# Optimization experiments

Hardware: AMD Instinct MI355X
Metric: run time of the kernel (lower is better)

The kernel has to match this reference:

```python
import jax, jax.numpy as jnp
import numpy as np

NUM_HEADS = 8
GROUP = 16
LN_EPS = 1e-5

def _star_relu(x, scale, bias):
    return scale * jnp.square(jax.nn.relu(x)) + bias

def _layernorm(x, w, b):
    mu = x.mean(-1, keepdims=True)
    var = jnp.mean(jnp.square(x - mu), -1, keepdims=True)
    return (x - mu) / jnp.sqrt(var + LN_EPS) * w + b

def _attention(x, qkv_w, proj_w, proj_b, pa_scale, pa_bias, lf_w, lf_b, hf_w, hf_b, lf_gamma, hf_gamma):
    B, N, C = x.shape
    hd = C // NUM_HEADS
    detail = _star_relu(x, pa_scale, pa_bias)
    lf = jnp.tanh(detail @ lf_w.T + lf_b)                      # (B,N,H)
    hf = jax.nn.softplus(detail @ hf_w.T + hf_b)
    hf_sq = jnp.square(hf)
    hf = 2.0 * hf_sq / (hf_sq + 0.3678)
    lf = jnp.repeat(lf, hd, axis=-1)                           # (B,N,C): per-head value repeated across head_dim
    hf = jnp.repeat(hf, hd, axis=-1)
    qkv = (x @ qkv_w.T).reshape(B, N, 3, NUM_HEADS, hd).transpose(2, 0, 3, 1, 4)
    q, k, v = qkv[0], qkv[1], qkv[2]
    q = q * (hd ** -0.5)
    attn = jax.nn.softmax(jnp.einsum('bhqd,bhkd->bhqk', q, k), axis=-1)
    attn_out = jnp.einsum('bhqk,bhkd->bhqd', attn, v).transpose(0, 2, 1, 3).reshape(B, N, C)
    value_tokens = v.transpose(0, 2, 1, 3).reshape(B, N, C)
    high_res = value_tokens - attn_out
    attn_out = attn_out + attn_out * lf * lf_gamma + hf * high_res * hf_gamma
    return attn_out @ proj_w.T + proj_b

def _freq_scale(x, rw1_w, rw1_scale, rw1_bias, rw2_w, freq_w):
    # x: (B,C,H,W); freq_w: (num_filters, C//group, base_size, base_size//2+1) == rfft grid
    B, C, H, W = x.shape
    xf = jnp.fft.rfft2(x, axes=(2, 3), norm='ortho')           # (B,C,fh,fw) complex
    pooled = x.mean(axis=(2, 3))                               # (B,C)
    h = _star_relu(pooled @ rw1_w.T, rw1_scale, rw1_bias)
    routing = jnp.tanh((h @ rw2_w.T).reshape(B, GROUP, -1))    # (B,g,f)
    fh, fw = xf.shape[2], xf.shape[3]
    dyn = jnp.einsum('bgf,fchw->bgchw', routing, freq_w).reshape(B, C, fh, fw)
    xf = xf * dyn
    return jnp.fft.irfft2(xf, s=(H, W), axes=(2, 3), norm='ortho')

def _forward(x, norm1_w, norm1_b, qkv_w, proj_w, proj_b, pa_scale, pa_bias, lf_w, lf_b, hf_w, hf_b,
             lf_gamma, hf_gamma, fs1_rw1_w, fs1_rw1_scale, fs1_rw1_bias, fs1_rw2_w, fs1_fw, gamma_1,
             norm2_w, norm2_b, fc1_w, fc1_b, fc2_w, fc2_b, fs2_rw1_w, fs2_rw1_scale, fs2_rw1_bias,
             fs2_rw2_w, fs2_fw, gamma_2):
    B, C, H, W = x.shape
    tokens = x.reshape(B, C, H * W).transpose(0, 2, 1)         # nchw -> nlc
    att_tokens = _attention(_layernorm(tokens, norm1_w, norm1_b),
                            qkv_w, proj_w, proj_b, pa_scale, pa_bias,
                            lf_w, lf_b, hf_w, hf_b, lf_gamma, hf_gamma)
    att_feat = att_tokens.transpose(0, 2, 1).reshape(B, C, H, W)
    att_feat = _freq_scale(att_feat, fs1_rw1_w, fs1_rw1_scale, fs1_rw1_bias, fs1_rw2_w, fs1_fw) + att_feat
    att_tokens = att_feat.reshape(B, C, H * W).transpose(0, 2, 1)
    tokens = tokens + gamma_1 * att_tokens
    h = _layernorm(tokens, norm2_w, norm2_b)
    mlp_tokens = jax.nn.gelu(h @ fc1_w.T + fc1_b, approximate=False) @ fc2_w.T + fc2_b
    mlp_feat = mlp_tokens.transpose(0, 2, 1).reshape(B, C, H, W)
    mlp_feat = _freq_scale(mlp_feat, fs2_rw1_w, fs2_rw1_scale, fs2_rw1_bias, fs2_rw2_w, fs2_fw) + mlp_feat
    mlp_tokens = mlp_feat.reshape(B, C, H * W).transpose(0, 2, 1)
    tokens = tokens + gamma_2 * mlp_tokens
    return tokens.transpose(0, 2, 1).reshape(B, C, H, W)

def setup_inputs() -> dict:
    key = jax.random.key(0)
    ks = jax.random.split(key, 16)
    B, C, H, W = 16, 512, 32, 32
    heads, group, nf, bs = 8, 16, 4, 32
    hid_rw = int(C * 0.125)
    hid_mlp = int(C * 4.0)
    bfs = bs // 2 + 1
    d = {}
    d['x'] = jax.random.normal(ks[0], (B, C, H, W), jnp.float32)
    d['norm1_w'] = jnp.ones((C,), jnp.float32); d['norm1_b'] = jnp.zeros((C,), jnp.float32)
    d['qkv_w'] = jax.random.normal(ks[1], (3 * C, C), jnp.float32) * 0.02
    d['proj_w'] = jax.random.normal(ks[2], (C, C), jnp.float32) * 0.02
    d['proj_b'] = jnp.zeros((C,), jnp.float32)
    d['pa_scale'] = jnp.ones((1,), jnp.float32); d['pa_bias'] = jnp.zeros((1,), jnp.float32)
    d['lf_w'] = jax.random.normal(ks[3], (heads, C), jnp.float32) * 0.02
    d['lf_b'] = jnp.zeros((heads,), jnp.float32)
    d['hf_w'] = jax.random.normal(ks[4], (heads, C), jnp.float32) * 0.02
    d['hf_b'] = jnp.zeros((heads,), jnp.float32)
    d['lf_gamma'] = 1e-5 * jnp.ones((C,), jnp.float32)
    d['hf_gamma'] = 1e-5 * jnp.ones((C,), jnp.float32)
    d['fs1_rw1_w'] = jax.random.normal(ks[5], (hid_rw, C), jnp.float32) * 0.02
    d['fs1_rw1_scale'] = jnp.ones((1,), jnp.float32); d['fs1_rw1_bias'] = jnp.zeros((1,), jnp.float32)
    d['fs1_rw2_w'] = jax.random.normal(ks[6], (group * nf, hid_rw), jnp.float32) * 0.02
    d['fs1_fw'] = jax.random.normal(ks[7], (nf, C // group, bs, bfs), jnp.float32) * 1e-5
    d['gamma_1'] = 1e-4 * jnp.ones((C,), jnp.float32)
    d['norm2_w'] = jnp.ones((C,), jnp.float32); d['norm2_b'] = jnp.zeros((C,), jnp.float32)
    d['fc1_w'] = jax.random.normal(ks[8], (hid_mlp, C), jnp.float32) * 0.02
    d['fc1_b'] = jnp.zeros((hid_mlp,), jnp.float32)
    d['fc2_w'] = jax.random.normal(ks[9], (C, hid_mlp), jnp.float32) * 0.02
    d['fc2_b'] = jnp.zeros((C,), jnp.float32)
    d['fs2_rw1_w'] = jax.random.normal(ks[10], (hid_rw, C), jnp.float32) * 0.02
    d['fs2_rw1_scale'] = jnp.ones((1,), jnp.float32); d['fs2_rw1_bias'] = jnp.zeros((1,), jnp.float32)
    d['fs2_rw2_w'] = jax.random.normal(ks[11], (group * nf, hid_rw), jnp.float32) * 0.02
    d['fs2_fw'] = jax.random.normal(ks[12], (nf, C // group, bs, bfs), jnp.float32) * 1e-5
    d['gamma_2'] = 1e-4 * jnp.ones((C,), jnp.float32)
    return d

def reference(x, norm1_w, norm1_b, qkv_w, proj_w, proj_b, pa_scale, pa_bias, lf_w, lf_b, hf_w, hf_b,
              lf_gamma, hf_gamma, fs1_rw1_w, fs1_rw1_scale, fs1_rw1_bias, fs1_rw2_w, fs1_fw, gamma_1,
              norm2_w, norm2_b, fc1_w, fc1_b, fc2_w, fc2_b, fs2_rw1_w, fs2_rw1_scale, fs2_rw1_bias,
              fs2_rw2_w, fs2_fw, gamma_2):
    return _forward(x, norm1_w, norm1_b, qkv_w, proj_w, proj_b, pa_scale, pa_bias, lf_w, lf_b, hf_w, hf_b,
                    lf_gamma, hf_gamma, fs1_rw1_w, fs1_rw1_scale, fs1_rw1_bias, fs1_rw2_w, fs1_fw, gamma_1,
                    norm2_w, norm2_b, fc1_w, fc1_b, fc2_w, fc2_b, fs2_rw1_w, fs2_rw1_scale, fs2_rw1_bias,
                    fs2_rw2_w, fs2_fw, gamma_2)
```

## Files before the change

kernel.cpp:

```cpp
#include <hip/hip_runtime.h>
#include <cstdint>
#include <cstddef>

#define B_   16
#define C_   512
#define N_   1024
#define M_   (B_*N_)
#define NH_  8
#define HD_  64
#define C3_  1536
#define CH_  2048

typedef __attribute__((ext_vector_type(8))) short bf16x8;
typedef __attribute__((ext_vector_type(4))) float f32x4;
typedef __attribute__((ext_vector_type(4))) unsigned short u16x4;

__device__ __forceinline__ unsigned short f2bf(float f) {
  union { float f; unsigned u; } v; v.f = f;
  unsigned r = v.u + 0x7fffu + ((v.u >> 16) & 1u);
  return (unsigned short)(r >> 16);
}
__device__ __forceinline__ float bf2f(unsigned short h) {
  union { unsigned u; float f; } v; v.u = ((unsigned)h) << 16;
  return v.f;
}
__device__ __forceinline__ unsigned f2u(float f) {
  union { float f; unsigned u; } v; v.f = f; return v.u;
}

__global__ __launch_bounds__(256) void k_f2b4(
    const float* __restrict__ s0, unsigned short* __restrict__ d0,
    const float* __restrict__ s1, unsigned short* __restrict__ d1,
    const float* __restrict__ s2, unsigned short* __restrict__ d2,
    const float* __restrict__ s3, unsigned short* __restrict__ d3) {
  int blk = blockIdx.x, t = threadIdx.x;
  const float* s; unsigned short* d; int off;
  if (blk < 3072)      { s = s0; d = d0; off = blk * 256; }
  else if (blk < 4096) { s = s1; d = d1; off = (blk - 3072) * 256; }
  else if (blk < 8192) { s = s2; d = d2; off = (blk - 4096) * 256; }
  else                 { s = s3; d = d3; off = (blk - 8192) * 256; }
  int i = off + t;
  d[i] = f2bf(s[i]);
}

__global__ __launch_bounds__(256) void k_twid(unsigned short* __restrict__ gtab) {
  int idx = blockIdx.x * 256 + threadIdx.x;
  if (idx >= 6400) return;
  int tab = idx / 1280, rem = idx % 1280;
  int i = rem / 40, j = rem % 40;
  float v = 0.f;
  if (j < 32) {
    float th = 0.19634954084936207f * (float)((i * j) & 31);
    float s, c;
    __sincosf(th, &s, &c);
    if (tab == 0) v = c;
    else if (tab == 1) v = s;
    else if (tab == 2) v = -s;
    else {
      float wg = (j == 0 || j == 16) ? 1.f : 2.f;
      if (j >= 17) wg = 0.f;
      v = (tab == 3) ? wg * c : -wg * s;
    }
  }
  gtab[idx] = f2bf(v);
}

__global__ __launch_bounds__(256) void k_transpose_cn(const float* __restrict__ x,
                                                      float* __restrict__ tok) {
  __shared__ float s[32][33];
  const int n0 = blockIdx.x * 32, c0 = blockIdx.y * 32, b = blockIdx.z;
  const int j = threadIdx.x & 31, i0 = threadIdx.x >> 5;
  #pragma unroll
  for (int k = 0; k < 4; ++k) {
    int i = i0 + k * 8;
    s[i][j] = x[(size_t)(b * C_ + c0 + i) * N_ + n0 + j];
  }
  __syncthreads();
  #pragma unroll
  for (int k = 0; k < 4; ++k) {
    int i = i0 + k * 8;
    tok[(size_t)(b * N_ + n0 + i) * C_ + c0 + j] = s[j][i];
  }
}

template<bool WITH>
__global__ __launch_bounds__(256) void k_ln(const float* __restrict__ tok,
    const float* __restrict__ w, const float* __restrict__ bia,
    const float* __restrict__ lfw, const float* __restrict__ lfb,
    const float* __restrict__ hfw, const float* __restrict__ hfb,
    const float* __restrict__ pa_s, const float* __restrict__ pa_b,
    unsigned short* __restrict__ lnout, float* __restrict__ lfout,
    float* __restrict__ hfout) {
  const int t = threadIdx.x, wv = t >> 6, l = t & 63;
  const int row = blockIdx.x * 4 + wv;
  const float* p = tok + (size_t)row * C_;
  float v[8];
  *(float4*)&v[0] = *(const float4*)(p + 4 * l);
  *(float4*)&v[4] = *(const float4*)(p + 256 + 4 * l);
  float s = 0.f, q = 0.f;
  #pragma unroll
  for (int i = 0; i < 8; ++i) { s += v[i]; q += v[i] * v[i]; }
  #pragma unroll
  for (int off = 1; off < 64; off <<= 1) { s += __shfl_xor(s, off); q += __shfl_xor(q, off); }
  float mu = s * (1.f / 512.f);
  float var = q * (1.f / 512.f) - mu * mu;
  float rstd = rsqrtf(var + 1e-5f);
  float wv8[8], bv8[8];
  *(float4*)&wv8[0] = *(const float4*)(w + 4 * l);
  *(float4*)&wv8[4] = *(const float4*)(w + 256 + 4 * l);
  *(float4*)&bv8[0] = *(const float4*)(bia + 4 * l);
  *(float4*)&bv8[4] = *(const float4*)(bia + 256 + 4 * l);
  float ln[8];
  #pragma unroll
  for (int i = 0; i < 8; ++i) ln[i] = (v[i] - mu) * rstd * wv8[i] + bv8[i];
  u16x4 o0 = { f2bf(ln[0]), f2bf(ln[1]), f2bf(ln[2]), f2bf(ln[3]) };
  u16x4 o1 = { f2bf(ln[4]), f2bf(ln[5]), f2bf(ln[6]), f2bf(ln[7]) };
  *(u16x4*)(lnout + (size_t)row * C_ + 4 * l) = o0;
  *(u16x4*)(lnout + (size_t)row * C_ + 256 + 4 * l) = o1;
  if (WITH) {
    float ps = pa_s[0], pb = pa_b[0];
    float d[8];
    #pragma unroll
    for (int i = 0; i < 8; ++i) { float r = fmaxf(ln[i], 0.f); d[i] = ps * r * r + pb; }
    float lacc[8], hacc[8];
    #pragma unroll
    for (int h = 0; h < 8; ++h) {
      float lw[8], hw[8];
      *(float4*)&lw[0] = *(const float4*)(lfw + h * C_ + 4 * l);
      *(float4*)&lw[4] = *(const float4*)(lfw + h * C_ + 256 + 4 * l);
      *(float4*)&hw[0] = *(const float4*)(hfw + h * C_ + 4 * l);
      *(float4*)&hw[4] = *(const float4*)(hfw + h * C_ + 256 + 4 * l);
      float la = 0.f, ha = 0.f;
      #pragma unroll
      for (int i = 0; i < 8; ++i) { la += d[i] * lw[i]; ha += d[i] * hw[i]; }
      lacc[h] = la; hacc[h] = ha;
    }
    #pragma unroll
    for (int h = 0; h < 8; ++h)
      #pragma unroll
      for (int off = 1; off < 64; off <<= 1) {
        lacc[h] += __shfl_xor(lacc[h], off);
        hacc[h] += __shfl_xor(hacc[h], off);
      }
    float lv = lacc[0], hv = hacc[0];
    #pragma unroll
    for (int h = 1; h < 8; ++h) { if (l == h) { lv = lacc[h]; hv = hacc[h]; } }
    if (l < 8) {
      lfout[(size_t)row * 8 + l] = tanhf(lv + lfb[l]);
      float z = hv + hfb[l];
      float sp = (z > 15.f) ? z : log1pf(__expf(z));
      float s2 = sp * sp;
      hfout[(size_t)row * 8 + l] = 2.f * s2 / (s2 + 0.3678f);
    }
  }
}

template<int EPI>
__global__ __launch_bounds__(256) void k_gemm(const unsigned short* __restrict__ A,
    const unsigned short* __restrict__ Bt, const float* __restrict__ bias,
    void* __restrict__ outv, unsigned short* __restrict__ vtg, int Nn, int K) {
  __shared__ __align__(16) unsigned short Asm[128 * 40];
  __shared__ __align__(16) unsigned short Bsm[128 * 40];
  const int t = threadIdx.x, w = t >> 6, l = t & 63;
  const int lane15 = l & 15, quad = l >> 4;
  const int n0 = blockIdx.x * 128, m0 = blockIdx.y * 128;
  const int wm = w >> 1, wn = w & 1;
  f32x4 acc[4][4];
  #pragma unroll
  for (int i = 0; i < 4; ++i)
    #pragma unroll
    for (int j = 0; j < 4; ++j) acc[i][j] = (f32x4){0.f, 0.f, 0.f, 0.f};
  const int sr = t >> 2, sc = (t & 3) * 8;
  const unsigned short* Ab = A + (size_t)(m0 + sr) * K + sc;
  const unsigned short* Bb = Bt + (size_t)(n0 + sr) * K + sc;
  const size_t rstep = (size_t)64 * K;
  bf16x8 ga0 = *(const bf16x8*)Ab;
  bf16x8 ga1 = *(const bf16x8*)(Ab + rstep);
  bf16x8 gb0 = *(const bf16x8*)Bb;
  bf16x8 gb1 = *(const bf16x8*)(Bb + rstep);
  for (int k0 = 0; k0 < K; k0 += 32) {
    __syncthreads();
    *(bf16x8*)&Asm[sr * 40 + sc] = ga0;
    *(bf16x8*)&Asm[(sr + 64) * 40 + sc] = ga1;
    *(bf16x8*)&Bsm[sr * 40 + sc] = gb0;
    *(bf16x8*)&Bsm[(sr + 64) * 40 + sc] = gb1;
    __syncthreads();
    if (k0 + 32 < K) {
      ga0 = *(const bf16x8*)(Ab + k0 + 32);
      ga1 = *(const bf16x8*)(Ab + rstep + k0 + 32);
      gb0 = *(const bf16x8*)(Bb + k0 + 32);
      gb1 = *(const bf16x8*)(Bb + rstep + k0 + 32);
    }
    bf16x8 af[4], bg[4];
    #pragma unroll
    for (int i = 0; i < 4; ++i)
      af[i] = *(const bf16x8*)&Asm[(wm * 64 + i * 16 + lane15) * 40 + quad * 8];
    #pragma unroll
    for (int i = 0; i < 4; ++i)
      bg[i] = *(const bf16x8*)&Bsm[(wn * 64 + i * 16 + lane15) * 40 + quad * 8];
    #pragma unroll
    for (int i = 0; i < 4; ++i)
      #pragma unroll
      for (int j = 0; j < 4; ++j)
        acc[i][j] = __builtin_amdgcn_mfma_f32_16x16x32_bf16(af[i], bg[j], acc[i][j], 0, 0, 0);
  }
  #pragma unroll
  for (int i = 0; i < 4; ++i) {
    int grow = m0 + wm * 64 + i * 16 + quad * 4;
    int bq = grow >> 10, nq = grow & 1023;
    #pragma unroll
    for (int j = 0; j < 4; ++j) {
      int gcol = n0 + wn * 64 + j * 16 + lane15;
      float bs = (EPI == 0) ? 0.f : bias[gcol];
      if (EPI == 1 || EPI == 3) {
        float4 o = make_float4(acc[i][j][0] + bs, acc[i][j][1] + bs,
                               acc[i][j][2] + bs, acc[i][j][3] + bs);
        *(float4*)&((float*)outv)[((size_t)(bq * C_ + gcol) << 10) + nq] = o;
      } else if (EPI == 0) {
        u16x4 pv;
        #pragma unroll
        for (int r = 0; r < 4; ++r) {
          unsigned short hv = f2bf(acc[i][j][r]);
          pv[r] = hv;
          ((unsigned short*)outv)[(size_t)(grow + r) * Nn + gcol] = hv;
        }
        if (gcol >= 1024)
          *(u16x4*)&vtg[((size_t)(bq * C_ + gcol - 1024) << 10) + nq] = pv;
      } else {
        #pragma unroll
        for (int r = 0; r < 4; ++r) {
          float vv = acc[i][j][r] + bs;
          float e = __builtin_amdgcn_exp2f(-(2.302118073f * vv +
                                             0.1029455568f * vv * vv * vv));
          float g = vv * __builtin_amdgcn_rcpf(1.f + e);
          ((unsigned short*)outv)[(size_t)(grow + r) * Nn + gcol] = f2bf(g);
        }
      }
    }
  }
}

__global__ __launch_bounds__(256) void k_flash(const unsigned short* __restrict__ qkv,
    const unsigned short* __restrict__ vtg, const float* __restrict__ lf,
    const float* __restrict__ hf, const float* __restrict__ lgam,
    const float* __restrict__ hgam, unsigned short* __restrict__ y) {
  const int t = threadIdx.x, w = t >> 6, l = t & 63;
  const int lane15 = l & 15, quad = l >> 4;
  const int q0 = blockIdx.x * 64;
  const int h = blockIdx.y, b = blockIdx.z;
  __shared__ __align__(16) unsigned short kt[128 * 72];
  __shared__ __align__(16) unsigned short vt[64 * 136];
  __shared__ __align__(16) unsigned short pl[4][16 * 72];

  bf16x8 aq0, aq1;
  {
    const unsigned short* qp = qkv + (size_t)(b * N_ + q0 + w * 16 + lane15) * C3_ + h * 64 + quad * 8;
    bf16x8 r0 = *(const bf16x8*)qp;
    bf16x8 r1 = *(const bf16x8*)(qp + 32);
    #pragma unroll
    for (int i = 0; i < 8; ++i) {
      aq0[i] = (short)f2bf(0.1803368801111713f * bf2f((unsigned short)r0[i]));
      aq1[i] = (short)f2bf(0.1803368801111713f * bf2f((unsigned short)r1[i]));
    }
  }
  f32x4 O[4];
  #pragma unroll
  for (int i = 0; i < 4; ++i) O[i] = (f32x4){0.f, 0.f, 0.f, 0.f};
  float lsum = 0.f;

  const int sr = t >> 3;
  const int sc = (t & 7) * 8;
  const unsigned short* kb = qkv + (size_t)(b * N_ + sr) * C3_ + 512 + h * 64 + sc;
  const unsigned short* vb = vtg + (size_t)((b * NH_ + h) * HD_ + sr) * N_ + sc;
  bf16x8 gk0 = *(const bf16x8*)kb;
  bf16x8 gk1 = *(const bf16x8*)(kb + (size_t)32 * C3_);
  bf16x8 gk2 = *(const bf16x8*)(kb + (size_t)64 * C3_);
  bf16x8 gk3 = *(const bf16x8*)(kb + (size_t)96 * C3_);
  bf16x8 gv0 = *(const bf16x8*)vb;
  bf16x8 gv1 = *(const bf16x8*)(vb + 64);
  bf16x8 gv2 = *(const bf16x8*)(vb + 32 * N_);
  bf16x8 gv3 = *(const bf16x8*)(vb + 32 * N_ + 64);

  for (int kti = 0; kti < 8; ++kti) {
    __syncthreads();
    *(bf16x8*)&kt[sr * 72 + sc] = gk0;
    *(bf16x8*)&kt[(sr + 32) * 72 + sc] = gk1;
    *(bf16x8*)&kt[(sr + 64) * 72 + sc] = gk2;
    *(bf16x8*)&kt[(sr + 96) * 72 + sc] = gk3;
    *(bf16x8*)&vt[sr * 136 + sc] = gv0;
    *(bf16x8*)&vt[sr * 136 + 64 + sc] = gv1;
    *(bf16x8*)&vt[(sr + 32) * 136 + sc] = gv2;
    *(bf16x8*)&vt[(sr + 32) * 136 + 64 + sc] = gv3;
    __syncthreads();
    if (kti < 7) {
      const unsigned short* kn = kb + (size_t)((kti + 1) * 128) * C3_;
      const unsigned short* vn = vb + (kti + 1) * 128;
      gk0 = *(const bf16x8*)kn;
      gk1 = *(const bf16x8*)(kn + (size_t)32 * C3_);
      gk2 = *(const bf16x8*)(kn + (size_t)64 * C3_);
      gk3 = *(const bf16x8*)(kn + (size_t)96 * C3_);
      gv0 = *(const bf16x8*)vn;
      gv1 = *(const bf16x8*)(vn + 64);
      gv2 = *(const bf16x8*)(vn + 32 * N_);
      gv3 = *(const bf16x8*)(vn + 32 * N_ + 64);
    }

    #pragma unroll
    for (int half = 0; half < 2; ++half) {
      f32x4 S[4];
      #pragma unroll
      for (int nt = 0; nt < 4; ++nt) {
        const int nrow = half * 64 + nt * 16 + lane15;
        bf16x8 ak0 = *(const bf16x8*)&kt[nrow * 72 + quad * 8];
        bf16x8 ak1 = *(const bf16x8*)&kt[nrow * 72 + 32 + quad * 8];
        f32x4 z = (f32x4){0.f, 0.f, 0.f, 0.f};
        z = __builtin_amdgcn_mfma_f32_16x16x32_bf16(ak0, aq0, z, 0, 0, 0);
        z = __builtin_amdgcn_mfma_f32_16x16x32_bf16(ak1, aq1, z, 0, 0, 0);
        S[nt] = z;
      }
      #pragma unroll
      for (int nt = 0; nt < 4; ++nt)
        #pragma unroll
        for (int r = 0; r < 4; ++r) {
          float pv = __builtin_amdgcn_exp2f(S[nt][r]);
          S[nt][r] = pv;
          lsum += pv;
        }
      #pragma unroll
      for (int nt = 0; nt < 4; ++nt) {
        unsigned lo = __builtin_amdgcn_perm(f2u(S[nt][1]), f2u(S[nt][0]), 0x07060302u);
        unsigned hi = __builtin_amdgcn_perm(f2u(S[nt][3]), f2u(S[nt][2]), 0x07060302u);
        uint2 pk = make_uint2(lo, hi);
        *(uint2*)&pl[w][lane15 * 72 + nt * 16 + quad * 4] = pk;
      }
      #pragma unroll
      for (int nc = 0; nc < 2; ++nc) {
        bf16x8 ap = *(const bf16x8*)&pl[w][lane15 * 72 + nc * 32 + quad * 8];
        #pragma unroll
        for (int dt = 0; dt < 4; ++dt) {
          bf16x8 bv = *(const bf16x8*)&vt[(dt * 16 + lane15) * 136 + half * 64 + nc * 32 + quad * 8];
          O[dt] = __builtin_amdgcn_mfma_f32_16x16x32_bf16(ap, bv, O[dt], 0, 0, 0);
        }
      }
    }
  }

  lsum += __shfl_xor(lsum, 16);
  lsum += __shfl_xor(lsum, 32);
  float inv = 1.f / lsum;
  float invr[4], lfr[4], hfr[4];
  #pragma unroll
  for (int r = 0; r < 4; ++r) {
    invr[r] = __shfl(inv, quad * 4 + r);
    int grow = b * N_ + q0 + w * 16 + quad * 4 + r;
    lfr[r] = lf[grow * 8 + h];
    hfr[r] = hf[grow * 8 + h];
  }
  const size_t rowb = (size_t)(b * N_ + q0 + w * 16 + quad * 4);
  #pragma unroll
  for (int dt = 0; dt < 4; ++dt) {
    int cc = h * 64 + dt * 16 + lane15;
    float lg = lgam[cc], hg = hgam[cc];
    #pragma unroll
    for (int r = 0; r < 4; ++r) {
      float a = O[dt][r] * invr[r];
      float vval = bf2f(qkv[(rowb + r) * C3_ + 1024 + cc]);
      float res = a + a * lfr[r] * lg + hfr[r] * (vval - a) * hg;
      y[(rowb + r) * C_ + cc] = f2bf(res);
    }
  }
}

__global__ __launch_bounds__(256) void k_pool(const float* __restrict__ feat,
                                              float* __restrict__ pooled) {
  int row = blockIdx.x * 4 + (threadIdx.x >> 6);
  int l = threadIdx.x & 63;
  const float4* p = (const float4*)(feat + (size_t)row * N_);
  float4 a = p[l], b4 = p[l + 64], c4 = p[l + 128], d4 = p[l + 192];
  float s = a.x + a.y + a.z + a.w + b4.x + b4.y + b4.z + b4.w +
            c4.x + c4.y + c4.z + c4.w + d4.x + d4.y + d4.z + d4.w;
  #pragma unroll
  for (int off = 1; off < 64; off <<= 1) s += __shfl_xor(s, off);
  if (l == 0) pooled[row] = s * (1.f / 1024.f);
}

__global__ __launch_bounds__(256) void k_routing(const float* __restrict__ pooled,
    const float* __restrict__ rw1, const float* __restrict__ rw1s,
    const float* __restrict__ rw1b, const float* __restrict__ rw2,
    float* __restrict__ routing) {
  const int b = blockIdx.x, t = threadIdx.x;
  __shared__ float plds[512];
  __shared__ float tile[64][65];
  __shared__ float hl[64];
  plds[t] = pooled[b * 512 + t];
  plds[t + 256] = pooled[b * 512 + t + 256];
  __syncthreads();
  float acc = 0.f;
  for (int c0 = 0; c0 < 512; c0 += 64) {
    #pragma unroll
    for (int kk = 0; kk < 16; ++kk) {
      int idx = kk * 256 + t;
      tile[idx >> 6][idx & 63] = rw1[(size_t)(idx >> 6) * 512 + c0 + (idx & 63)];
    }
    __syncthreads();
    if (t < 64) {
      #pragma unroll
      for (int i = 0; i < 64; ++i) acc += plds[c0 + i] * tile[t][i];
    }
    __syncthreads();
  }
  if (t < 64) {
    float r = fmaxf(acc, 0.f);
    hl[t] = rw1s[0] * r * r + rw1b[0];
  }
  __syncthreads();
  if (t < 64) {
    float r2 = 0.f;
    #pragma unroll
    for (int j = 0; j < 64; ++j) r2 += hl[j] * rw2[(size_t)t * 64 + j];
    routing[b * 64 + t] = tanhf(r2);
  }
}

__global__ __launch_bounds__(256) void k_freq(const float* __restrict__ feat,
    const float* __restrict__ routing, const float* __restrict__ fwtab,
    const unsigned short* __restrict__ gtab, float* __restrict__ enh) {
  const int c = blockIdx.x, b = blockIdx.y, t = threadIdx.x;
  const int g = c >> 5, cc = c & 31;
  const int w = t >> 6, l = t & 63;
  const int lane15 = l & 15, quad = l >> 4;
  const int mt = w & 1, nt = w >> 1;
  __shared__ __align__(16) unsigned short Xbf[32 * 40];
  __shared__ __align__(16) float p[32 * 36];
  __shared__ __align__(16) unsigned short Tabs[6400];
  __shared__ __align__(16) unsigned short pl1r[32 * 40], pl1i[32 * 40];
  __shared__ __align__(16) unsigned short pl2r[32 * 40], pl2i[32 * 40];
  __shared__ __align__(16) unsigned short pl3r[32 * 40], pl3i[32 * 40];
  __shared__ float Ms[1024];
  const size_t base = (size_t)(b * C_ + c) * N_;

  {
    float4 v = ((const float4*)(feat + base))[t];
    int hh = t >> 3, w4 = (t & 7) * 4;
    *(float4*)&p[hh * 36 + w4] = v;
    u16x4 xb = { f2bf(v.x), f2bf(v.y), f2bf(v.z), f2bf(v.w) };
    *(u16x4*)&Xbf[hh * 40 + w4] = xb;
  }
  {
    const uint4* src = (const uint4*)gtab;
    uint4* dst = (uint4*)Tabs;
    #pragma unroll
    for (int k = 0; k < 4; ++k) {
      int o = k * 256 + t;
      if (o < 800) dst[o] = src[o];
    }
  }
  {
    float r0 = routing[b * 64 + g * 4 + 0];
    float r1 = routing[b * 64 + g * 4 + 1];
    float r2 = routing[b * 64 + g * 4 + 2];
    float r3 = routing[b * 64 + g * 4 + 3];
    const float* fb = fwtab + (size_t)cc * 544;
    #pragma unroll
    for (int k = 0; k < 4; ++k) {
      int o = k * 256 + t;
      int fh = o >> 5, fw = o & 31;
      float mv = 0.f;
      if (fw < 17) {
        int fi = fh * 17 + fw;
        mv = (r0 * fb[fi] + r1 * fb[17408 + fi] + r2 * fb[34816 + fi] +
              r3 * fb[52224 + fi]) * (1.f / 1024.f);
      }
      Ms[o] = mv;
    }
  }
  __syncthreads();

  const unsigned short* Tc  = Tabs;
  const unsigned short* Ts  = Tabs + 1280;
  const unsigned short* Tsn = Tabs + 2560;
  const unsigned short* Tcw = Tabs + 3840;
  const unsigned short* Tsw = Tabs + 5120;
  const int arow = (mt * 16 + lane15) * 40 + quad * 8;
  const int brow = (nt * 16 + lane15) * 40 + quad * 8;
  const int prow = (nt * 16 + lane15) * 40 + mt * 16 + quad * 4;
  const f32x4 zz = (f32x4){0.f, 0.f, 0.f, 0.f};

  {
    bf16x8 aX = *(const bf16x8*)&Xbf[arow];
    bf16x8 bC = *(const bf16x8*)&Tc[brow];
    bf16x8 bS = *(const bf16x8*)&Tsn[brow];
    f32x4 re = __builtin_amdgcn_mfma_f32_16x16x32_bf16(aX, bC, zz, 0, 0, 0);
    f32x4 im = __builtin_amdgcn_mfma_f32_16x16x32_bf16(aX, bS, zz, 0, 0, 0);
    uint2 pr = make_uint2(__builtin_amdgcn_perm(f2u(re[1]), f2u(re[0]), 0x07060302u),
                          __builtin_amdgcn_perm(f2u(re[3]), f2u(re[2]), 0x07060302u));
    uint2 pi = make_uint2(__builtin_amdgcn_perm(f2u(im[1]), f2u(im[0]), 0x07060302u),
                          __builtin_amdgcn_perm(f2u(im[3]), f2u(im[2]), 0x07060302u));
    *(uint2*)&pl1r[prow] = pr;
    *(uint2*)&pl1i[prow] = pi;
  }
  __syncthreads();
  {
    bf16x8 aC = *(const bf16x8*)&Tc[arow];
    bf16x8 aS = *(const bf16x8*)&Ts[arow];
    bf16x8 aN = *(const bf16x8*)&Tsn[arow];
    bf16x8 bR = *(const bf16x8*)&pl1r[brow];
    bf16x8 bI = *(const bf16x8*)&pl1i[brow];
    f32x4 er = __builtin_amdgcn_mfma_f32_16x16x32_bf16(aC, bR, zz, 0, 0, 0);
    er = __builtin_amdgcn_mfma_f32_16x16x32_bf16(aS, bI, er, 0, 0, 0);
    f32x4 ei = __builtin_amdgcn_mfma_f32_16x16x32_bf16(aC, bI, zz, 0, 0, 0);
    ei = __builtin_amdgcn_mfma_f32_16x16x32_bf16(aN, bR, ei, 0, 0, 0);
    #pragma unroll
    for (int r = 0; r < 4; ++r) {
      float mk = Ms[(mt * 16 + quad * 4 + r) * 32 + nt * 16 + lane15];
      er[r] *= mk; ei[r] *= mk;
    }
    uint2 pr = make_uint2(__builtin_amdgcn_perm(f2u(er[1]), f2u(er[0]), 0x07060302u),
                          __builtin_amdgcn_perm(f2u(er[3]), f2u(er[2]), 0x07060302u));
    uint2 pi = make_uint2(__builtin_amdgcn_perm(f2u(ei[1]), f2u(ei[0]), 0x07060302u),
                          __builtin_amdgcn_perm(f2u(ei[3]), f2u(ei[2]), 0x07060302u));
    *(uint2*)&pl2r[prow] = pr;
    *(uint2*)&pl2i[prow] = pi;
  }
  __syncthreads();
  {
    bf16x8 aR = *(const bf16x8*)&pl2r[arow];
    bf16x8 aI = *(const bf16x8*)&pl2i[arow];
    bf16x8 bC = *(const bf16x8*)&Tc[brow];
    bf16x8 bS = *(const bf16x8*)&Ts[brow];
    bf16x8 bN = *(const bf16x8*)&Tsn[brow];
    f32x4 zr = __builtin_amdgcn_mfma_f32_16x16x32_bf16(aR, bC, zz, 0, 0, 0);
    zr = __builtin_amdgcn_mfma_f32_16x16x32_bf16(aI, bN, zr, 0, 0, 0);
    f32x4 zi = __builtin_amdgcn_mfma_f32_16x16x32_bf16(aI, bC, zz, 0, 0, 0);
    zi = __builtin_amdgcn_mfma_f32_16x16x32_bf16(aR, bS, zi, 0, 0, 0);
    uint2 pr = make_uint2(__builtin_amdgcn_perm(f2u(zr[1]), f2u(zr[0]), 0x07060302u),
                          __builtin_amdgcn_perm(f2u(zr[3]), f2u(zr[2]), 0x07060302u));
    uint2 pi = make_uint2(__builtin_amdgcn_perm(f2u(zi[1]), f2u(zi[0]), 0x07060302u),
                          __builtin_amdgcn_perm(f2u(zi[3]), f2u(zi[2]), 0x07060302u));
    *(uint2*)&pl3r[prow] = pr;
    *(uint2*)&pl3i[prow] = pi;
  }
  __syncthreads();
  {
    bf16x8 aC = *(const bf16x8*)&Tcw[arow];
    bf16x8 aS = *(const bf16x8*)&Tsw[arow];
    bf16x8 bR = *(const bf16x8*)&pl3r[brow];
    bf16x8 bI = *(const bf16x8*)&pl3i[brow];
    f32x4 y = __builtin_amdgcn_mfma_f32_16x16x32_bf16(aC, bR, zz, 0, 0, 0);
    y = __builtin_amdgcn_mfma_f32_16x16x32_bf16(aS, bI, y, 0, 0, 0);
    int hh = nt * 16 + lane15, w0 = mt * 16 + quad * 4;
    float4 res = *(const float4*)&p[hh * 36 + w0];
    float4 o = make_float4(y[0] + res.x, y[1] + res.y, y[2] + res.z, y[3] + res.w);
    *(float4*)&enh[base + hh * 32 + w0] = o;
  }
}

__global__ __launch_bounds__(256) void k_add_t(const float* __restrict__ enh,
    const float* __restrict__ gamma, float* __restrict__ tok) {
  __shared__ float s[32][33];
  const int n0 = blockIdx.x * 32, c0 = blockIdx.y * 32, b = blockIdx.z;
  const int j = threadIdx.x & 31, i0 = threadIdx.x >> 5;
  #pragma unroll
  for (int k = 0; k < 4; ++k) {
    int i = i0 + k * 8;
    s[i][j] = enh[(size_t)(b * C_ + c0 + i) * N_ + n0 + j];
  }
  __syncthreads();
  float gv = gamma[c0 + j];
  #pragma unroll
  for (int k = 0; k < 4; ++k) {
    int i = i0 + k * 8;
    size_t o = (size_t)(b * N_ + n0 + i) * C_ + c0 + j;
    tok[o] += gv * s[j][i];
  }
}

__global__ __launch_bounds__(256) void k_final(const float* __restrict__ tok,
    const float* __restrict__ gamma, const float* __restrict__ enh,
    float* __restrict__ out) {
  __shared__ float s[32][33];
  const int n0 = blockIdx.x * 32, c0 = blockIdx.y * 32, b = blockIdx.z;
  const int j = threadIdx.x & 31, i0 = threadIdx.x >> 5;
  #pragma unroll
  for (int k = 0; k < 4; ++k) {
    int i = i0 + k * 8;
    s[i][j] = tok[(size_t)(b * N_ + n0 + i) * C_ + c0 + j];
  }
  __syncthreads();
  #pragma unroll
  for (int k = 0; k < 4; ++k) {
    int i = i0 + k * 8;
    size_t o = (size_t)(b * C_ + c0 + i) * N_ + n0 + j;
    out[o] = s[j][i] + gamma[c0 + i] * enh[o];
  }
}

extern "C" void kernel_launch(void* const* d_in, const int* in_sizes, int n_in,
                              void* d_out, int out_size, void* d_ws, size_t ws_size,
                              hipStream_t stream) {
  (void)in_sizes; (void)n_in; (void)out_size; (void)ws_size;
  const float* x      = (const float*)d_in[0];
  const float* n1w    = (const float*)d_in[1];
  const float* n1b    = (const float*)d_in[2];
  const float* qkv_w  = (const float*)d_in[3];
  const float* proj_w = (const float*)d_in[4];
  const float* proj_b = (const float*)d_in[5];
  const float* pa_s   = (const float*)d_in[6];
  const float* pa_b   = (const float*)d_in[7];
  const float* lf_w   = (const float*)d_in[8];
  const float* lf_b   = (const float*)d_in[9];
  const float* hf_w   = (const float*)d_in[10];
  const float* hf_b   = (const float*)d_in[11];
  const float* lf_g   = (const float*)d_in[12];
  const float* hf_g   = (const float*)d_in[13];
  const float* f1rw1w = (const float*)d_in[14];
  const float* f1rw1s = (const float*)d_in[15];
  const float* f1rw1b = (const float*)d_in[16];
  const float* f1rw2w = (const float*)d_in[17];
  const float* f1fw   = (const float*)d_in[18];
  const float* gamma1 = (const float*)d_in[19];
  const float* n2w    = (const float*)d_in[20];
  const float* n2b    = (const float*)d_in[21];
  const float* fc1w   = (const float*)d_in[22];
  const float* fc1b   = (const float*)d_in[23];
  const float* fc2w   = (const float*)d_in[24];
  const float* fc2b   = (const float*)d_in[25];
  const float* f2rw1w = (const float*)d_in[26];
  const float* f2rw1s = (const float*)d_in[27];
  const float* f2rw1b = (const float*)d_in[28];
  const float* f2rw2w = (const float*)d_in[29];
  const float* f2fw   = (const float*)d_in[30];
  const float* gamma2 = (const float*)d_in[31];

  char* ws = (char*)d_ws;
  float*          tokens = (float*)(ws + 0);
  float*          f1buf  = (float*)(ws + 33554432ULL);
  float*          f2buf  = (float*)(ws + 67108864ULL);
  float*          f3buf  = (float*)(ws + 100663296ULL);
  unsigned short* regA   = (unsigned short*)(ws + 134217728ULL);
  unsigned short* abuf   = (unsigned short*)(ws + 201326592ULL);
  float*          lfbuf  = (float*)(ws + 218103808ULL);
  float*          hfbuf  = (float*)(ws + 218628096ULL);
  float*          pooled = (float*)(ws + 219152384ULL);
  float*          routing= (float*)(ws + 219185152ULL);
  unsigned short* wq     = (unsigned short*)(ws + 219189248ULL);
  unsigned short* wp     = (unsigned short*)(ws + 220762112ULL);
  unsigned short* w1     = (unsigned short*)(ws + 221286400ULL);
  unsigned short* w2     = (unsigned short*)(ws + 223383552ULL);
  unsigned short* gtab   = (unsigned short*)(ws + 225480704ULL);
  unsigned short* vtg    = (unsigned short*)f1buf;

  k_f2b4<<<12288, 256, 0, stream>>>(qkv_w, wq, proj_w, wp, fc1w, w1, fc2w, w2);
  k_twid<<<25, 256, 0, stream>>>(gtab);

  k_transpose_cn<<<dim3(32, 16, 16), 256, 0, stream>>>(x, tokens);
  k_ln<true><<<4096, 256, 0, stream>>>(tokens, n1w, n1b, lf_w, lf_b, hf_w, hf_b,
                                       pa_s, pa_b, abuf, lfbuf, hfbuf);
  k_gemm<0><<<dim3(12, 128), 256, 0, stream>>>(abuf, wq, n1b, regA, vtg, C3_, C_);
  k_flash<<<dim3(16, 8, 16), 256, 0, stream>>>(regA, vtg, lfbuf, hfbuf, lf_g, hf_g, abuf);
  k_gemm<1><<<dim3(4, 128), 256, 0, stream>>>(abuf, wp, proj_b, f2buf, nullptr, C_, C_);
  k_pool<<<2048, 256, 0, stream>>>(f2buf, pooled);
  k_routing<<<16, 256, 0, stream>>>(pooled, f1rw1w, f1rw1s, f1rw1b, f1rw2w, routing);
  k_freq<<<dim3(512, 16), 256, 0, stream>>>(f2buf, routing, f1fw, gtab, f3buf);
  k_add_t<<<dim3(32, 16, 16), 256, 0, stream>>>(f3buf, gamma1, tokens);
  k_ln<false><<<4096, 256, 0, stream>>>(tokens, n2w, n2b, nullptr, nullptr, nullptr,
                                        nullptr, nullptr, nullptr, abuf, nullptr, nullptr);
  k_gemm<2><<<dim3(16, 128), 256, 0, stream>>>(abuf, w1, fc1b, regA, nullptr, CH_, C_);
  k_gemm<3><<<dim3(4, 128), 256, 0, stream>>>(regA, w2, fc2b, f2buf, nullptr, C_, CH_);
  k_pool<<<2048, 256, 0, stream>>>(f2buf, pooled);
  k_routing<<<16, 256, 0, stream>>>(pooled, f2rw1w, f2rw1s, f2rw1b, f2rw2w, routing);
  k_freq<<<dim3(512, 16), 256, 0, stream>>>(f2buf, routing, f2fw, gtab, f3buf);
  k_final<<<dim3(32, 16, 16), 256, 0, stream>>>(tokens, gamma2, f3buf, (float*)d_out);
}
```

Before: 548.9 us.

## Keep residual stream in channel-major layout and fuse transposes into LN and freq kernels

```diff
diff --git a/kernel.cpp b/kernel.cpp
--- a/kernel.cpp
+++ b/kernel.cpp
@@ -65,92 +65,86 @@
   gtab[idx] = f2bf(v);
 }
 
-__global__ __launch_bounds__(256) void k_transpose_cn(const float* __restrict__ x,
-                                                      float* __restrict__ tok) {
-  __shared__ float s[32][33];
-  const int n0 = blockIdx.x * 32, c0 = blockIdx.y * 32, b = blockIdx.z;
-  const int j = threadIdx.x & 31, i0 = threadIdx.x >> 5;
-  #pragma unroll
-  for (int k = 0; k < 4; ++k) {
-    int i = i0 + k * 8;
-    s[i][j] = x[(size_t)(b * C_ + c0 + i) * N_ + n0 + j];
-  }
-  __syncthreads();
-  #pragma unroll
-  for (int k = 0; k < 4; ++k) {
-    int i = i0 + k * 8;
-    tok[(size_t)(b * N_ + n0 + i) * C_ + c0 + j] = s[j][i];
-  }
-}
-
 template<bool WITH>
-__global__ __launch_bounds__(256) void k_ln(const float* __restrict__ tok,
+__global__ __launch_bounds__(256) void k_lnt(const float* __restrict__ src,
     const float* __restrict__ w, const float* __restrict__ bia,
     const float* __restrict__ lfw, const float* __restrict__ lfb,
     const float* __restrict__ hfw, const float* __restrict__ hfb,
     const float* __restrict__ pa_s, const float* __restrict__ pa_b,
     unsigned short* __restrict__ lnout, float* __restrict__ lfout,
     float* __restrict__ hfout) {
+  __shared__ unsigned short s[512 * 34];
   const int t = threadIdx.x, wv = t >> 6, l = t & 63;
-  const int row = blockIdx.x * 4 + wv;
-  const float* p = tok + (size_t)row * C_;
-  float v[8];
-  *(float4*)&v[0] = *(const float4*)(p + 4 * l);
-  *(float4*)&v[4] = *(const float4*)(p + 256 + 4 * l);
-  float s = 0.f, q = 0.f;
-  #pragma unroll
-  for (int i = 0; i < 8; ++i) { s += v[i]; q += v[i] * v[i]; }
-  #pragma unroll
-  for (int off = 1; off < 64; off <<= 1) { s += __shfl_xor(s, off); q += __shfl_xor(q, off); }
-  float mu = s * (1.f / 512.f);
-  float var = q * (1.f / 512.f) - mu * mu;
-  float rstd = rsqrtf(var + 1e-5f);
+  const int n0 = blockIdx.x * 32, b = blockIdx.y;
+  const int cl = t >> 3;
+  const int nn = (t & 7) * 4;
+  #pragma unroll
+  for (int k = 0; k < 16; ++k) {
+    int c = k * 32 + cl;
+    float4 v = *(const float4*)&src[(size_t)(b * C_ + c) * N_ + n0 + nn];
+    s[c * 34 + nn]     = f2bf(v.x);
+    s[c * 34 + nn + 1] = f2bf(v.y);
+    s[c * 34 + nn + 2] = f2bf(v.z);
+    s[c * 34 + nn + 3] = f2bf(v.w);
+  }
+  __syncthreads();
   float wv8[8], bv8[8];
-  *(float4*)&wv8[0] = *(const float4*)(w + 4 * l);
-  *(float4*)&wv8[4] = *(const float4*)(w + 256 + 4 * l);
-  *(float4*)&bv8[0] = *(const float4*)(bia + 4 * l);
-  *(float4*)&bv8[4] = *(const float4*)(bia + 256 + 4 * l);
-  float ln[8];
-  #pragma unroll
-  for (int i = 0; i < 8; ++i) ln[i] = (v[i] - mu) * rstd * wv8[i] + bv8[i];
-  u16x4 o0 = { f2bf(ln[0]), f2bf(ln[1]), f2bf(ln[2]), f2bf(ln[3]) };
-  u16x4 o1 = { f2bf(ln[4]), f2bf(ln[5]), f2bf(ln[6]), f2bf(ln[7]) };
-  *(u16x4*)(lnout + (size_t)row * C_ + 4 * l) = o0;
-  *(u16x4*)(lnout + (size_t)row * C_ + 256 + 4 * l) = o1;
-  if (WITH) {
-    float ps = pa_s[0], pb = pa_b[0];
-    float d[8];
-    #pragma unroll
-    for (int i = 0; i < 8; ++i) { float r = fmaxf(ln[i], 0.f); d[i] = ps * r * r + pb; }
-    float lacc[8], hacc[8];
-    #pragma unroll
-    for (int h = 0; h < 8; ++h) {
-      float lw[8], hw[8];
-      *(float4*)&lw[0] = *(const float4*)(lfw + h * C_ + 4 * l);
-      *(float4*)&lw[4] = *(const float4*)(lfw + h * C_ + 256 + 4 * l);
-      *(float4*)&hw[0] = *(const float4*)(hfw + h * C_ + 4 * l);
-      *(float4*)&hw[4] = *(const float4*)(hfw + h * C_ + 256 + 4 * l);
-      float la = 0.f, ha = 0.f;
-      #pragma unroll
-      for (int i = 0; i < 8; ++i) { la += d[i] * lw[i]; ha += d[i] * hw[i]; }
-      lacc[h] = la; hacc[h] = ha;
-    }
-    #pragma unroll
-    for (int h = 0; h < 8; ++h)
-      #pragma unroll
-      for (int off = 1; off < 64; off <<= 1) {
-        lacc[h] += __shfl_xor(lacc[h], off);
-        hacc[h] += __shfl_xor(hacc[h], off);
+  #pragma unroll
+  for (int k = 0; k < 8; ++k) { wv8[k] = w[l + 64 * k]; bv8[k] = bia[l + 64 * k]; }
+  float ps = 1.f, pb = 0.f;
+  if (WITH) { ps = pa_s[0]; pb = pa_b[0]; }
+  for (int ri = 0; ri < 8; ++ri) {
+    const int n = wv * 8 + ri;
+    const int row = b * N_ + n0 + n;
+    float v[8];
+    #pragma unroll
+    for (int k = 0; k < 8; ++k) v[k] = bf2f(s[(l + 64 * k) * 34 + n]);
+    float sm = 0.f, q = 0.f;
+    #pragma unroll
+    for (int k = 0; k < 8; ++k) { sm += v[k]; q += v[k] * v[k]; }
+    #pragma unroll
+    for (int off = 1; off < 64; off <<= 1) { sm += __shfl_xor(sm, off); q += __shfl_xor(q, off); }
+    float mu = sm * (1.f / 512.f);
+    float var = q * (1.f / 512.f) - mu * mu;
+    float rstd = rsqrtf(var + 1e-5f);
+    float ln[8];
+    #pragma unroll
+    for (int k = 0; k < 8; ++k) ln[k] = (v[k] - mu) * rstd * wv8[k] + bv8[k];
+    #pragma unroll
+    for (int k = 0; k < 8; ++k)
+      lnout[(size_t)row * C_ + l + 64 * k] = f2bf(ln[k]);
+    if (WITH) {
+      float d[8];
+      #pragma unroll
+      for (int k = 0; k < 8; ++k) { float r = fmaxf(ln[k], 0.f); d[k] = ps * r * r + pb; }
+      float lacc[8], hacc[8];
+      #pragma unroll
+      for (int h = 0; h < 8; ++h) {
+        float la = 0.f, ha = 0.f;
+        #pragma unroll
+        for (int k = 0; k < 8; ++k) {
+          la += d[k] * lfw[h * C_ + l + 64 * k];
+          ha += d[k] * hfw[h * C_ + l + 64 * k];
+        }
+        lacc[h] = la; hacc[h] = ha;
       }
-    float lv = lacc[0], hv = hacc[0];
-    #pragma unroll
-    for (int h = 1; h < 8; ++h) { if (l == h) { lv = lacc[h]; hv = hacc[h]; } }
-    if (l < 8) {
-      lfout[(size_t)row * 8 + l] = tanhf(lv + lfb[l]);
-      float z = hv + hfb[l];
-      float sp = (z > 15.f) ? z : log1pf(__expf(z));
-      float s2 = sp * sp;
-      hfout[(size_t)row * 8 + l] = 2.f * s2 / (s2 + 0.3678f);
+      #pragma unroll
+      for (int h = 0; h < 8; ++h)
+        #pragma unroll
+        for (int off = 1; off < 64; off <<= 1) {
+          lacc[h] += __shfl_xor(lacc[h], off);
+          hacc[h] += __shfl_xor(hacc[h], off);
+        }
+      float lv = lacc[0], hv = hacc[0];
+      #pragma unroll
+      for (int h = 1; h < 8; ++h) { if (l == h) { lv = lacc[h]; hv = hacc[h]; } }
+      if (l < 8) {
+        lfout[(size_t)row * 8 + l] = tanhf(lv + lfb[l]);
+        float z = hv + hfb[l];
+        float sp = (z > 15.f) ? z : log1pf(__expf(z));
+        float s2 = sp * sp;
+        hfout[(size_t)row * 8 + l] = 2.f * s2 / (s2 + 0.3678f);
+      }
     }
   }
 }
@@ -424,7 +418,8 @@
 
 __global__ __launch_bounds__(256) void k_freq(const float* __restrict__ feat,
     const float* __restrict__ routing, const float* __restrict__ fwtab,
-    const unsigned short* __restrict__ gtab, float* __restrict__ enh) {
+    const unsigned short* __restrict__ gtab, const float* __restrict__ res,
+    const float* __restrict__ gamma, float* __restrict__ outp) {
   const int c = blockIdx.x, b = blockIdx.y, t = threadIdx.x;
   const int g = c >> 5, cc = c & 31;
   const int w = t >> 6, l = t & 63;
@@ -549,49 +544,12 @@
     f32x4 y = __builtin_amdgcn_mfma_f32_16x16x32_bf16(aC, bR, zz, 0, 0, 0);
     y = __builtin_amdgcn_mfma_f32_16x16x32_bf16(aS, bI, y, 0, 0, 0);
     int hh = nt * 16 + lane15, w0 = mt * 16 + quad * 4;
-    float4 res = *(const float4*)&p[hh * 36 + w0];
-    float4 o = make_float4(y[0] + res.x, y[1] + res.y, y[2] + res.z, y[3] + res.w);
-    *(float4*)&enh[base + hh * 32 + w0] = o;
-  }
-}
-
-__global__ __launch_bounds__(256) void k_add_t(const float* __restrict__ enh,
-    const float* __restrict__ gamma, float* __restrict__ tok) {
-  __shared__ float s[32][33];
-  const int n0 = blockIdx.x * 32, c0 = blockIdx.y * 32, b = blockIdx.z;
-  const int j = threadIdx.x & 31, i0 = threadIdx.x >> 5;
-  #pragma unroll
-  for (int k = 0; k < 4; ++k) {
-    int i = i0 + k * 8;
-    s[i][j] = enh[(size_t)(b * C_ + c0 + i) * N_ + n0 + j];
-  }
-  __syncthreads();
-  float gv = gamma[c0 + j];
-  #pragma unroll
-  for (int k = 0; k < 4; ++k) {
-    int i = i0 + k * 8;
-    size_t o = (size_t)(b * N_ + n0 + i) * C_ + c0 + j;
-    tok[o] += gv * s[j][i];
-  }
-}
-
-__global__ __launch_bounds__(256) void k_final(const float* __restrict__ tok,
-    const float* __restrict__ gamma, const float* __restrict__ enh,
-    float* __restrict__ out) {
-  __shared__ float s[32][33];
-  const int n0 = blockIdx.x * 32, c0 = blockIdx.y * 32, b = blockIdx.z;
-  const int j = threadIdx.x & 31, i0 = threadIdx.x >> 5;
-  #pragma unroll
-  for (int k = 0; k < 4; ++k) {
-    int i = i0 + k * 8;
-    s[i][j] = tok[(size_t)(b * N_ + n0 + i) * C_ + c0 + j];
-  }
-  __syncthreads();
-  #pragma unroll
-  for (int k = 0; k < 4; ++k) {
-    int i = i0 + k * 8;
-    size_t o = (size_t)(b * C_ + c0 + i) * N_ + n0 + j;
-    out[o] = s[j][i] + gamma[c0 + i] * enh[o];
+    float4 fp = *(const float4*)&p[hh * 36 + w0];
+    float4 rp = *(const float4*)&res[base + hh * 32 + w0];
+    float gv = gamma[c];
+    float4 o = make_float4(rp.x + gv * (y[0] + fp.x), rp.y + gv * (y[1] + fp.y),
+                           rp.z + gv * (y[2] + fp.z), rp.w + gv * (y[3] + fp.w));
+    *(float4*)&outp[base + hh * 32 + w0] = o;
   }
 }
 
@@ -636,7 +594,6 @@
   float*          tokens = (float*)(ws + 0);
   float*          f1buf  = (float*)(ws + 33554432ULL);
   float*          f2buf  = (float*)(ws + 67108864ULL);
-  float*          f3buf  = (float*)(ws + 100663296ULL);
   unsigned short* regA   = (unsigned short*)(ws + 134217728ULL);
   unsigned short* abuf   = (unsigned short*)(ws + 201326592ULL);
   float*          lfbuf  = (float*)(ws + 218103808ULL);
@@ -653,22 +610,21 @@
   k_f2b4<<<12288, 256, 0, stream>>>(qkv_w, wq, proj_w, wp, fc1w, w1, fc2w, w2);
   k_twid<<<25, 256, 0, stream>>>(gtab);
 
-  k_transpose_cn<<<dim3(32, 16, 16), 256, 0, stream>>>(x, tokens);
-  k_ln<true><<<4096, 256, 0, stream>>>(tokens, n1w, n1b, lf_w, lf_b, hf_w, hf_b,
-                                       pa_s, pa_b, abuf, lfbuf, hfbuf);
+  k_lnt<true><<<dim3(32, 16), 256, 0, stream>>>(x, n1w, n1b, lf_w, lf_b, hf_w, hf_b,
+                                                pa_s, pa_b, abuf, lfbuf, hfbuf);
   k_gemm<0><<<dim3(12, 128), 256, 0, stream>>>(abuf, wq, n1b, regA, vtg, C3_, C_);
   k_flash<<<dim3(16, 8, 16), 256, 0, stream>>>(regA, vtg, lfbuf, hfbuf, lf_g, hf_g, abuf);
   k_gemm<1><<<dim3(4, 128), 256, 0, stream>>>(abuf, wp, proj_b, f2buf, nullptr, C_, C_);
   k_pool<<<2048, 256, 0, stream>>>(f2buf, pooled);
   k_routing<<<16, 256, 0, stream>>>(pooled, f1rw1w, f1rw1s, f1rw1b, f1rw2w, routing);
-  k_freq<<<dim3(512, 16), 256, 0, stream>>>(f2buf, routing, f1fw, gtab, f3buf);
-  k_add_t<<<dim3(32, 16, 16), 256, 0, stream>>>(f3buf, gamma1, tokens);
-  k_ln<false><<<4096, 256, 0, stream>>>(tokens, n2w, n2b, nullptr, nullptr, nullptr,
-                                        nullptr, nullptr, nullptr, abuf, nullptr, nullptr);
+  k_freq<<<dim3(512, 16), 256, 0, stream>>>(f2buf, routing, f1fw, gtab, x, gamma1, tokens);
+  k_lnt<false><<<dim3(32, 16), 256, 0, stream>>>(tokens, n2w, n2b, nullptr, nullptr,
+                                                 nullptr, nullptr, nullptr, nullptr,
+                                                 abuf, nullptr, nullptr);
   k_gemm<2><<<dim3(16, 128), 256, 0, stream>>>(abuf, w1, fc1b, regA, nullptr, CH_, C_);
   k_gemm<3><<<dim3(4, 128), 256, 0, stream>>>(regA, w2, fc2b, f2buf, nullptr, C_, CH_);
   k_pool<<<2048, 256, 0, stream>>>(f2buf, pooled);
   k_routing<<<16, 256, 0, stream>>>(pooled, f2rw1w, f2rw1s, f2rw1b, f2rw2w, routing);
-  k_freq<<<dim3(512, 16), 256, 0, stream>>>(f2buf, routing, f2fw, gtab, f3buf);
-  k_final<<<dim3(32, 16, 16), 256, 0, stream>>>(tokens, gamma2, f3buf, (float*)d_out);
-}
+  k_freq<<<dim3(512, 16), 256, 0, stream>>>(f2buf, routing, f2fw, gtab, tokens, gamma2,
+                                            (float*)d_out);
+}
```

Result: faster. 522.3 us (-4.8%).
